# Optimization experiments

Measured on AMD Instinct MI355X. Metric: run time of the kernel, lower is better.

The kernel has to match this reference:

```python
import jax, jax.numpy as jnp
import numpy as np

B, L, H, D = 4096, 256, 32, 2
LOG_PROB_FACTOR = 0.5

def setup_inputs() -> dict:
    key = jax.random.key(0)
    k0, k1, k2, k3 = jax.random.split(key, 4)
    x = jax.random.randint(k0, (B, L), 0, D)  # spin configs in {0,1}
    Wi = jax.random.normal(k1, (D, 4 * H), dtype=jnp.float32) * 0.1   # input kernel (no bias, flax LSTMCell)
    Wh = jax.random.normal(k2, (H, 4 * H), dtype=jnp.float32) * 0.1   # recurrent kernel
    bh = jnp.zeros((4 * H,), dtype=jnp.float32)                        # recurrent bias
    Wo = jax.random.normal(k3, (H, D), dtype=jnp.float32) * 0.1       # output Dense kernel
    bo = jnp.zeros((D,), dtype=jnp.float32)                            # output Dense bias
    return {"x": x, "Wi": Wi, "Wh": Wh, "bh": bh, "Wo": Wo, "bo": bo}

def reference(x, Wi, Wh, bh, Wo, bo):
    # one-hot of spin t-1 (zeros at t=0); log-prob is read out at spin t.
    x_oh = jax.nn.one_hot(x, D, dtype=Wi.dtype)      # [B, L, D]
    xs = jnp.swapaxes(x_oh, 0, 1)                    # [L, B, D] time-major for scan
    c0 = jnp.zeros((x.shape[0], H), Wi.dtype)
    h0 = jnp.zeros((x.shape[0], H), Wi.dtype)
    inp0 = jnp.zeros((x.shape[0], D), Wi.dtype)      # jnp.zeros(inputDim) initial input

    def step(carry, xt):
        c, h, inp = carry
        gates = inp @ Wi + h @ Wh + bh               # [B, 4H]
        i, f, g, o = jnp.split(gates, 4, axis=-1)    # flax LSTMCell gate order i,f,g,o
        c_new = jax.nn.sigmoid(f) * c + jax.nn.sigmoid(i) * jnp.tanh(g)
        h_new = jax.nn.sigmoid(o) * jnp.tanh(c_new)
        out = jax.nn.elu(h_new @ Wo + bo)            # Dense + actFun, [B, D]
        # log(sum(softmax(out) * onehot)) == gathered log_softmax (stable form)
        logp = jnp.sum(jax.nn.log_softmax(out, axis=-1) * xt, axis=-1)  # [B]
        return (c_new, h_new, xt), logp

    _, logps = jax.lax.scan(step, (c0, h0, inp0), xs)  # logps: [L, B]
    return LOG_PROB_FACTOR * jnp.sum(logps, axis=0)    # [B]
```

## Files before the change

kernel.cpp:

```cpp
#include <hip/hip_runtime.h>


typedef __attribute__((ext_vector_type(8))) short bf16x8;
typedef __attribute__((ext_vector_type(4))) float f32x4;

#define LOG2E 1.4426950408889634f
#define LN2   0.6931471805599453f

__device__ __forceinline__ float fexp2(float x) { return __builtin_amdgcn_exp2f(x); }
__device__ __forceinline__ float flog2(float x) { return __builtin_amdgcn_logf(x); }
__device__ __forceinline__ float frcp(float x)  { return __builtin_amdgcn_rcpf(x); }

__device__ __forceinline__ float fsig(float x)   { return frcp(1.f + fexp2(-LOG2E * x)); }
__device__ __forceinline__ float ftanh_(float x) { return 1.f - 2.f * frcp(fexp2(2.f * LOG2E * x) + 1.f); }
__device__ __forceinline__ float felu(float x)   { return x > 0.f ? x : fexp2(LOG2E * x) - 1.f; }

__device__ __forceinline__ unsigned short f2bf(float f) {
    unsigned u = __builtin_bit_cast(unsigned, f);
    u = (u + 0x7FFFu + ((u >> 16) & 1u)) >> 16;
    return (unsigned short)u;
}

__device__ __forceinline__ unsigned cvtpk_bf16(float a, float b) {
    unsigned r;
    asm("v_cvt_pk_bf16_f32 %0, %1, %2" : "=v"(r) : "v"(a), "v"(b));
    return r;
}

constexpr int Bsz = 4096;

__global__ __launch_bounds__(512, 1) void lstm_r20(
    const int*   __restrict__ x,
    const float* __restrict__ Wi,
    const float* __restrict__ Wh,
    const float* __restrict__ bh,
    const float* __restrict__ Wo,
    const float* __restrict__ bo,
    float*       __restrict__ out)
{
    const int tid  = threadIdx.x;
    const int w    = tid >> 6;
    const int lane = tid & 63;
    const int m    = lane & 15;
    const int oct  = lane >> 4;
    const int b0   = blockIdx.x * 16;

    __shared__ char   spinT[16][260];
    __shared__ float2 Sbuf[256][16];
    __shared__ short  hbuf[2][16][40];
    __shared__ float  red[32][16];

    {
        const int bl = tid >> 5;
        const int c8 = (tid & 31) * 8;
        const int4* src = reinterpret_cast<const int4*>(x + (b0 + bl) * 256 + c8);
        const int4 v0 = src[0], v1 = src[1];
        const int p0 = (v0.x & 1) | ((v0.y & 1) << 8) | ((v0.z & 1) << 16) | ((v0.w & 1) << 24);
        const int p1 = (v1.x & 1) | ((v1.y & 1) << 8) | ((v1.z & 1) << 16) | ((v1.w & 1) << 24);
        *reinterpret_cast<int*>(&spinT[bl][c8])     = p0;
        *reinterpret_cast<int*>(&spinT[bl][c8 + 4]) = p1;
    }

    bf16x8 wfrag;
    {
        const int r = m & 3;
        const float gs = (r == 2) ? 2.f * LOG2E : -LOG2E;
        const int colg = 32 * r + 4 * w + (m >> 2);
#pragma unroll
        for (int j = 0; j < 8; ++j)
            wfrag[j] = (short)f2bf(gs * Wh[(8 * oct + j) * 128 + colg]);
    }
    bf16x8 wfragO;
#pragma unroll
    for (int j = 0; j < 8; ++j)
        wfragO[j] = (m < 2) ? (short)f2bf(Wo[(8 * oct + j) * 2 + m]) : (short)0;

    const int u = 4 * w + oct;
    float bv0[4], bvd[4];
#pragma unroll
    for (int r = 0; r < 4; ++r) {
        const float gs = (r == 2) ? 2.f * LOG2E : -LOG2E;
        const int c0 = 32 * r + u;
        bv0[r] = gs * (bh[c0] + Wi[c0]);
        bvd[r] = gs * (Wi[128 + c0] - Wi[c0]);
    }
    const float bo0 = bo[0], bo1 = bo[1];

    float c = fsig(bh[u]) * ftanh_(bh[64 + u]);
    hbuf[0][m][u] = (short)f2bf(fsig(bh[96 + u]) * ftanh_(c));
    __syncthreads();

    const int wS = __builtin_amdgcn_readfirstlane(w);
    const f32x4 zero4 = { 0.f, 0.f, 0.f, 0.f };

    auto step = [&](const int t, const int rb, const int wb, const float spf) {
        const bf16x8 hfrag =
            *reinterpret_cast<const bf16x8*>(&hbuf[rb][m][8 * oct]);

        f32x4 cb;
#pragma unroll
        for (int r = 0; r < 4; ++r) cb[r] = fmaf(spf, bvd[r], bv0[r]);

        const f32x4 acc =
            __builtin_amdgcn_mfma_f32_16x16x32_bf16(wfrag, hfrag, cb, 0, 0, 0);

        const float ei = fexp2(acc[0]), ef = fexp2(acc[1]);
        const float eg = fexp2(acc[2]), eo = fexp2(acc[3]);
        const float P = (1.f + ei) * (1.f + eg);
        const float Q = 1.f + ef;
        const float R = frcp(P * Q);
        c = fmaf(P * R, c, (eg - 1.f) * Q * R);
        const float ec = fexp2(2.f * LOG2E * c);
        const float h  = (ec - 1.f) * frcp((1.f + eo) * (1.f + ec));
        hbuf[wb][m][u] = (short)cvtpk_bf16(h, h);

        if (wS == ((t - 1) & 7)) {
            const f32x4 aO =
                __builtin_amdgcn_mfma_f32_16x16x32_bf16(wfragO, hfrag, zero4, 0, 0, 0);
            if (oct == 0) Sbuf[t - 1][m] = make_float2(aO[0], aO[1]);
        }
        __syncthreads();
    };

    unsigned sp4 = *reinterpret_cast<const unsigned*>(&spinT[m][0]);
    for (int tb = 1; tb < 253; tb += 4) {
        const unsigned sp4n =
            *reinterpret_cast<const unsigned*>(&spinT[m][tb + 3]);
        step(tb,     0, 1, (float)(sp4 & 0xFFu));
        step(tb + 1, 1, 0, (float)((sp4 >> 8) & 0xFFu));
        step(tb + 2, 0, 1, (float)((sp4 >> 16) & 0xFFu));
        step(tb + 3, 1, 0, (float)(sp4 >> 24));
        sp4 = sp4n;
    }
    step(253, 0, 1, (float)(sp4 & 0xFFu));
    step(254, 1, 0, (float)((sp4 >> 8) & 0xFFu));
    step(255, 0, 1, (float)((sp4 >> 16) & 0xFFu));

    if (wS == 7) {
        const bf16x8 hfrag = *reinterpret_cast<const bf16x8*>(&hbuf[1][m][8 * oct]);
        const f32x4 aO =
            __builtin_amdgcn_mfma_f32_16x16x32_bf16(wfragO, hfrag, zero4, 0, 0, 0);
        if (oct == 0) Sbuf[255][m] = make_float2(aO[0], aO[1]);
    }
    __syncthreads();

    float lp = 0.f;
    {
        const int bpost = tid & 15;
        const int tc    = tid >> 4;
#pragma unroll
        for (int i = 0; i < 8; ++i) {
            const int t = tc * 8 + i;
            const float2 sv = Sbuf[t][bpost];
            const int sp = spinT[bpost][t];
            const float o0 = felu(sv.x + bo0);
            const float o1 = felu(sv.y + bo1);
            const float mx = fmaxf(o0, o1), mn = fminf(o0, o1);
            const float lse = mx + LN2 * flog2(1.f + fexp2(LOG2E * (mn - mx)));
            lp += (sp ? o1 : o0) - lse;
        }
        red[tc][bpost] = lp;
    }
    __syncthreads();
    if (tid < 16) {
        float s = 0.f;
#pragma unroll
        for (int tc2 = 0; tc2 < 32; ++tc2) s += red[tc2][tid];
        out[b0 + tid] = 0.5f * s;
    }
}

extern "C" void kernel_launch(void* const* d_in, const int* in_sizes, int n_in,
                              void* d_out, int out_size, void* d_ws, size_t ws_size,
                              hipStream_t stream) {
    const int*   x  = (const int*)d_in[0];
    const float* Wi = (const float*)d_in[1];
    const float* Wh = (const float*)d_in[2];
    const float* bh = (const float*)d_in[3];
    const float* Wo = (const float*)d_in[4];
    const float* bo = (const float*)d_in[5];
    float* out = (float*)d_out;

    lstm_r20<<<dim3(Bsz / 16), dim3(512), 0, stream>>>(x, Wi, Wh, bh, Wo, bo, out);
}
```

Baseline: 120.6 us.

## Add dedicated ninth wave for output projection, off the recurrence critical path

Adds a ninth wavefront per block that computes only the output-dense MFMA for the previous step's hidden state. Before, one of the eight recurrence waves did this each step in rotation. The eight gate waves now do only the LSTM cell update, which takes the extra MFMA off the critical path of each serialized step. The hidden buffer row is padded from 40 to 44 shorts and read as two 8-byte loads, likely to reduce LDS bank conflicts. In exchange the block grows to 576 threads, so every per-step barrier must sync one more wave.

```diff
diff --git a/kernel.cpp b/kernel.cpp
--- a/kernel.cpp
+++ b/kernel.cpp
@@ -2,6 +2,7 @@
 
 
 typedef __attribute__((ext_vector_type(8))) short bf16x8;
+typedef __attribute__((ext_vector_type(4))) short bf16x4;
 typedef __attribute__((ext_vector_type(4))) float f32x4;
 
 #define LOG2E 1.4426950408889634f
@@ -29,7 +30,7 @@
 
 constexpr int Bsz = 4096;
 
-__global__ __launch_bounds__(512, 1) void lstm_r20(
+__global__ __launch_bounds__(576, 1) void lstm_r21(
     const int*   __restrict__ x,
     const float* __restrict__ Wi,
     const float* __restrict__ Wh,
@@ -47,10 +48,10 @@
 
     __shared__ char   spinT[16][260];
     __shared__ float2 Sbuf[256][16];
-    __shared__ short  hbuf[2][16][40];
+    __shared__ __align__(16) short hbuf[2][16][44];
     __shared__ float  red[32][16];
 
-    {
+    if (w < 8) {
         const int bl = tid >> 5;
         const int c8 = (tid & 31) * 8;
         const int4* src = reinterpret_cast<const int4*>(x + (b0 + bl) * 256 + c8);
@@ -61,11 +62,12 @@
         *reinterpret_cast<int*>(&spinT[bl][c8 + 4]) = p1;
     }
 
+    const int wc = (w < 8) ? w : 0;
     bf16x8 wfrag;
     {
         const int r = m & 3;
         const float gs = (r == 2) ? 2.f * LOG2E : -LOG2E;
-        const int colg = 32 * r + 4 * w + (m >> 2);
+        const int colg = 32 * r + 4 * wc + (m >> 2);
 #pragma unroll
         for (int j = 0; j < 8; ++j)
             wfrag[j] = (short)f2bf(gs * Wh[(8 * oct + j) * 128 + colg]);
@@ -75,7 +77,7 @@
     for (int j = 0; j < 8; ++j)
         wfragO[j] = (m < 2) ? (short)f2bf(Wo[(8 * oct + j) * 2 + m]) : (short)0;
 
-    const int u = 4 * w + oct;
+    const int u = 4 * wc + oct;
     float bv0[4], bvd[4];
 #pragma unroll
     for (int r = 0; r < 4; ++r) {
@@ -86,35 +88,44 @@
     }
     const float bo0 = bo[0], bo1 = bo[1];
 
-    float c = fsig(bh[u]) * ftanh_(bh[64 + u]);
-    hbuf[0][m][u] = (short)f2bf(fsig(bh[96 + u]) * ftanh_(c));
+    float c = 0.f;
+    if (w < 8) {
+        c = fsig(bh[u]) * ftanh_(bh[64 + u]);
+        hbuf[0][m][u] = (short)f2bf(fsig(bh[96 + u]) * ftanh_(c));
+    }
     __syncthreads();
 
     const int wS = __builtin_amdgcn_readfirstlane(w);
     const f32x4 zero4 = { 0.f, 0.f, 0.f, 0.f };
 
+    auto loadh = [&](const int rb) -> bf16x8 {
+        const bf16x4 h0 = *reinterpret_cast<const bf16x4*>(&hbuf[rb][m][8 * oct]);
+        const bf16x4 h1 = *reinterpret_cast<const bf16x4*>(&hbuf[rb][m][8 * oct + 4]);
+        bf16x8 hf;
+#pragma unroll
+        for (int j = 0; j < 4; ++j) { hf[j] = h0[j]; hf[4 + j] = h1[j]; }
+        return hf;
+    };
+
     auto step = [&](const int t, const int rb, const int wb, const float spf) {
-        const bf16x8 hfrag =
-            *reinterpret_cast<const bf16x8*>(&hbuf[rb][m][8 * oct]);
-
-        f32x4 cb;
+        if (wS < 8) {
+            const bf16x8 hfrag = loadh(rb);
+            f32x4 cb;
 #pragma unroll
-        for (int r = 0; r < 4; ++r) cb[r] = fmaf(spf, bvd[r], bv0[r]);
-
-        const f32x4 acc =
-            __builtin_amdgcn_mfma_f32_16x16x32_bf16(wfrag, hfrag, cb, 0, 0, 0);
-
-        const float ei = fexp2(acc[0]), ef = fexp2(acc[1]);
-        const float eg = fexp2(acc[2]), eo = fexp2(acc[3]);
-        const float P = (1.f + ei) * (1.f + eg);
-        const float Q = 1.f + ef;
-        const float R = frcp(P * Q);
-        c = fmaf(P * R, c, (eg - 1.f) * Q * R);
-        const float ec = fexp2(2.f * LOG2E * c);
-        const float h  = (ec - 1.f) * frcp((1.f + eo) * (1.f + ec));
-        hbuf[wb][m][u] = (short)cvtpk_bf16(h, h);
-
-        if (wS == ((t - 1) & 7)) {
+            for (int r = 0; r < 4; ++r) cb[r] = fmaf(spf, bvd[r], bv0[r]);
+            const f32x4 acc =
+                __builtin_amdgcn_mfma_f32_16x16x32_bf16(wfrag, hfrag, cb, 0, 0, 0);
+            const float ei = fexp2(acc[0]), ef = fexp2(acc[1]);
+            const float eg = fexp2(acc[2]), eo = fexp2(acc[3]);
+            const float P = (1.f + ei) * (1.f + eg);
+            const float Q = 1.f + ef;
+            const float R = frcp(P * Q);
+            c = fmaf(P * R, c, (eg - 1.f) * Q * R);
+            const float ec = fexp2(2.f * LOG2E * c);
+            const float h  = (ec - 1.f) * frcp((1.f + eo) * (1.f + ec));
+            hbuf[wb][m][u] = (short)cvtpk_bf16(h, h);
+        } else {
+            const bf16x8 hfrag = loadh(rb);
             const f32x4 aO =
                 __builtin_amdgcn_mfma_f32_16x16x32_bf16(wfragO, hfrag, zero4, 0, 0, 0);
             if (oct == 0) Sbuf[t - 1][m] = make_float2(aO[0], aO[1]);
@@ -136,16 +147,16 @@
     step(254, 1, 0, (float)((sp4 >> 8) & 0xFFu));
     step(255, 0, 1, (float)((sp4 >> 16) & 0xFFu));
 
-    if (wS == 7) {
-        const bf16x8 hfrag = *reinterpret_cast<const bf16x8*>(&hbuf[1][m][8 * oct]);
+    if (wS == 8) {
+        const bf16x8 hfrag = loadh(1);
         const f32x4 aO =
             __builtin_amdgcn_mfma_f32_16x16x32_bf16(wfragO, hfrag, zero4, 0, 0, 0);
         if (oct == 0) Sbuf[255][m] = make_float2(aO[0], aO[1]);
     }
     __syncthreads();
 
-    float lp = 0.f;
-    {
+    if (tid < 512) {
+        float lp = 0.f;
         const int bpost = tid & 15;
         const int tc    = tid >> 4;
 #pragma unroll
@@ -181,5 +192,5 @@
     const float* bo = (const float*)d_in[5];
     float* out = (float*)d_out;
 
-    lstm_r20<<<dim3(Bsz / 16), dim3(512), 0, stream>>>(x, Wi, Wh, bh, Wo, bo, out);
+    lstm_r21<<<dim3(Bsz / 16), dim3(576), 0, stream>>>(x, Wi, Wh, bh, Wo, bo, out);
 }
```

Result: slower. 123.7 us (+2.5%).
